# Performance work log

Measured on AMD Instinct MI355X. Metric: run time of the kernel, lower is better.

Reference implementation:

```python
import jax, jax.numpy as jnp
import numpy as np

DIM = 192
NUM_HEADS = 6
KSZ = 7
MLP_RATIO = 4.0
LEVELS = 8
EPS = 1e-5


def layernorm(x, w, b):
    mu = jnp.mean(x, axis=-1, keepdims=True)
    var = jnp.mean(jnp.square(x - mu), axis=-1, keepdims=True)
    return (x - mu) * jax.lax.rsqrt(var + EPS) * w + b


def na2d(x, qkv_w, qkv_b, proj_w, proj_b, rpb):
    # Neighborhood attention 2D with relative position bias (NATTEN semantics:
    # window of KSZ x KSZ keys per query, clamped to stay inside the image).
    B, H, W, C = x.shape
    nh, hd = NUM_HEADS, C // NUM_HEADS
    scale = hd ** -0.5
    qkv = (x @ qkv_w.T + qkv_b).reshape(B, H, W, 3, nh, hd)
    q = qkv[..., 0, :, :] * scale  # [B,H,W,nh,hd]
    k = qkv[..., 1, :, :]
    v = qkv[..., 2, :, :]

    si = jnp.clip(jnp.arange(H) - KSZ // 2, 0, H - KSZ)
    idx_i = si[:, None] + jnp.arange(KSZ)  # [H,KSZ] row indices of each window
    sj = jnp.clip(jnp.arange(W) - KSZ // 2, 0, W - KSZ)
    idx_j = sj[:, None] + jnp.arange(KSZ)  # [W,KSZ]

    def gather_win(t):  # [B,H,W,nh,hd] -> [B,H,KSZ,W,KSZ,nh,hd]
        t = jnp.take(t, idx_i.reshape(-1), axis=1).reshape(B, H, KSZ, W, nh, hd)
        t = jnp.take(t, idx_j.reshape(-1), axis=3).reshape(B, H, KSZ, W, KSZ, nh, hd)
        return t

    kw = gather_win(k)
    vw = gather_win(v)

    # scores over the KSZ x KSZ neighborhood
    scores = jnp.einsum('bxynd,bxiyjnd->bxynij', q, kw)  # [B,H,W,nh,KSZ,KSZ]

    # relative position bias: rpb is [nh, 2K-1, 2K-1]
    rel_i = idx_i - jnp.arange(H)[:, None] + (KSZ - 1)  # [H,KSZ] in [0,2K-2]
    rel_j = idx_j - jnp.arange(W)[:, None] + (KSZ - 1)  # [W,KSZ]
    bias = rpb[:, rel_i][:, :, :, rel_j]  # [nh,H,KSZ,W,KSZ]
    scores = scores + bias.transpose(1, 3, 0, 2, 4)[None]

    attn = jax.nn.softmax(scores.reshape(B, H, W, nh, KSZ * KSZ), axis=-1)
    attn = attn.reshape(B, H, W, nh, KSZ, KSZ)
    out = jnp.einsum('bxynij,bxiyjnd->bxynd', attn, vw).reshape(B, H, W, C)
    return out @ proj_w.T + proj_b


def setup_inputs() -> dict:
    key = jax.random.key(0)
    ks = jax.random.split(key, 8)
    C = DIM
    hidden = int(C * MLP_RATIO)
    init = lambda k, shape: (jax.random.normal(k, shape, dtype=jnp.float32) * 0.02)
    return {
        'x': jax.random.normal(ks[0], (1, 128, 128, C), dtype=jnp.float32),
        'qkv_w': init(ks[1], (3 * C, C)),
        'qkv_b': jnp.zeros((3 * C,), jnp.float32),
        'proj_w': init(ks[2], (C, C)),
        'proj_b': jnp.zeros((C,), jnp.float32),
        'rpb': init(ks[3], (NUM_HEADS, 2 * KSZ - 1, 2 * KSZ - 1)),
        'ln1_w': jnp.ones((C,), jnp.float32),
        'ln1_b': jnp.zeros((C,), jnp.float32),
        'ln2_w': jnp.ones((C,), jnp.float32),
        'ln2_b': jnp.zeros((C,), jnp.float32),
        'fc1_w': init(ks[4], (hidden, C)),
        'fc1_b': jnp.zeros((hidden,), jnp.float32),
        'fc2_w': init(ks[5], (C, hidden)),
        'fc2_b': jnp.zeros((C,), jnp.float32),
        'gamma1': jnp.ones((LEVELS, C), jnp.float32),
        'gamma2': jnp.ones((LEVELS, C), jnp.float32),
        'quality': 4,
    }


def reference(x, qkv_w, qkv_b, proj_w, proj_b, rpb, ln1_w, ln1_b, ln2_w, ln2_b,
              fc1_w, fc1_b, fc2_w, fc2_b, gamma1, gamma2, quality):
    # eval-mode quality gating; quality is an integer so l = quality % 1 == 0
    s = int(quality) - 1
    g1 = jnp.abs(gamma1[s])
    g2 = jnp.abs(gamma2[s])

    shortcut = x
    h = layernorm(x, ln1_w, ln1_b)
    a = na2d(h, qkv_w, qkv_b, proj_w, proj_b, rpb)
    x = shortcut + g1 * a
    h2 = layernorm(x, ln2_w, ln2_b)
    m = jax.nn.gelu(h2 @ fc1_w.T + fc1_b, approximate=False) @ fc2_w.T + fc2_b
    x = x + g2 * m
    return x
```

## Files before the change

kernel.cpp:

```cpp
#include <hip/hip_runtime.h>
#include <hip/hip_bf16.h>
#include <math.h>

#define DIM 192
#define NHD 6
#define HD 32
#define KSZ 7
#define HID 768
#define IMH 128
#define IMW 128
#define NPIX (IMH*IMW)
#define WIN 14
#define KPAD 40

typedef __attribute__((ext_vector_type(8))) short short8;
typedef __attribute__((ext_vector_type(4))) float f32x4;

#define LDS_SYNC() do { \
    asm volatile("s_waitcnt lgkmcnt(0)" ::: "memory"); \
    __builtin_amdgcn_sched_barrier(0); \
    __builtin_amdgcn_s_barrier(); } while (0)

__global__ __launch_bounds__(256) void cvt_w(
    const float* __restrict__ qw, __hip_bfloat16* __restrict__ dq)
{
    int idx = blockIdx.x * 1024 + threadIdx.x * 4;
    float4 v4 = *(const float4*)(qw + idx);
    union { ushort4 u; __hip_bfloat16 h[4]; } o;
    o.h[0] = __float2bfloat16(v4.x); o.h[1] = __float2bfloat16(v4.y);
    o.h[2] = __float2bfloat16(v4.z); o.h[3] = __float2bfloat16(v4.w);
    *(ushort4*)&dq[idx] = o.u;
}

__device__ __forceinline__ void gl_lds16(const void* g, void* l) {
    __builtin_amdgcn_global_load_lds(
        (const __attribute__((address_space(1))) void*)g,
        (__attribute__((address_space(3))) void*)l, 16, 0, 0);
}

__device__ __forceinline__ short8 cvt8(float4 a, float4 b) {
    union { short8 v; __hip_bfloat16 h[8]; } u;
    u.h[0] = __float2bfloat16(a.x); u.h[1] = __float2bfloat16(a.y);
    u.h[2] = __float2bfloat16(a.z); u.h[3] = __float2bfloat16(a.w);
    u.h[4] = __float2bfloat16(b.x); u.h[5] = __float2bfloat16(b.y);
    u.h[6] = __float2bfloat16(b.z); u.h[7] = __float2bfloat16(b.w);
    return u.v;
}

__device__ __forceinline__ void stage_rows(const __hip_bfloat16* __restrict__ src,
                                           char* ldsbase, int wave, int lane) {
    int c0 = wave * 96 + lane;
    int r0 = c0 / 24, k0 = c0 - r0 * 24;
    gl_lds16(src + (size_t)r0 * DIM + ((k0 ^ (r0 & 7)) * 8), ldsbase + (wave * 96) * 16);
    int c1 = wave * 96 + 64 + (lane & 31);
    int r1 = c1 / 24, k1 = c1 - r1 * 24;
    if (lane < 32)
        gl_lds16(src + (size_t)r1 * DIM + ((k1 ^ (r1 & 7)) * 8), ldsbase + (wave * 96 + 64) * 16);
}
__device__ __forceinline__ void stage_w2(const __hip_bfloat16* __restrict__ W2, int ch,
                                         char* ldsbase, int wave, int lane) {
    int i0 = wave * 96 + lane;
    int r0 = i0 >> 3, o0 = i0 & 7;
    gl_lds16(W2 + (size_t)r0 * HID + ch * 64 + ((o0 ^ (r0 & 7)) * 8), ldsbase + (wave * 96) * 16);
    int i1 = wave * 96 + 64 + (lane & 31);
    int r1 = i1 >> 3, o1 = i1 & 7;
    if (lane < 32)
        gl_lds16(W2 + (size_t)r1 * HID + ch * 64 + ((o1 ^ (r1 & 7)) * 8), ldsbase + (wave * 96 + 64) * 16);
}

__global__ __launch_bounds__(256, 4) void qkv_ln_gemm(
    const float* __restrict__ x, const float* __restrict__ lnw, const float* __restrict__ lnb,
    const __hip_bfloat16* __restrict__ W, const float* __restrict__ bias,
    float* __restrict__ qb, __hip_bfloat16* __restrict__ kb, __hip_bfloat16* __restrict__ vb)
{
    __shared__ __hip_bfloat16 As[32 * 192];
    __shared__ __hip_bfloat16 Ws[64 * 192];
    int tid = threadIdx.x;
    int wave = tid >> 6, lane = tid & 63;
    int q = lane >> 4, col = lane & 15;
    int wm = (wave >> 1) * 16, wn = (wave & 1) * 32;
    int m0 = blockIdx.x * 32;

    auto stageW = [&](int ch) {
        #pragma unroll
        for (int i = 0; i < 6; i++) {
            int c = i * 256 + tid;
            int r = c / 24, kc = c - r * 24;
            gl_lds16(W + (size_t)(ch * 64 + r) * DIM + ((kc ^ (r & 7)) * 8),
                     (char*)&Ws[0] + (i * 256 + wave * 64) * 16);
        }
    };

    stageW(0);

    {
        int row = tid >> 3, sub = tid & 7;
        const float4* xr = (const float4*)(x + (size_t)(m0 + row) * DIM + sub * 24);
        float4 xa[6];
        float s = 0.f;
        #pragma unroll
        for (int i = 0; i < 6; i++) {
            xa[i] = xr[i];
            s += xa[i].x + xa[i].y + xa[i].z + xa[i].w;
        }
        s += __shfl_xor(s, 1); s += __shfl_xor(s, 2); s += __shfl_xor(s, 4);
        float mu = s * (1.0f / DIM);
        float qs = 0.f;
        #pragma unroll
        for (int i = 0; i < 6; i++) {
            float a = xa[i].x - mu, b = xa[i].y - mu, c = xa[i].z - mu, d = xa[i].w - mu;
            qs += a * a + b * b + c * c + d * d;
        }
        qs += __shfl_xor(qs, 1); qs += __shfl_xor(qs, 2); qs += __shfl_xor(qs, 4);
        float rstd = rsqrtf(qs * (1.0f / DIM) + 1e-5f);
        const float4* wv = (const float4*)(lnw + sub * 24);
        const float4* bv = (const float4*)(lnb + sub * 24);
        #pragma unroll
        for (int j = 0; j < 3; j++) {
            float4 v0 = xa[j * 2], v1 = xa[j * 2 + 1];
            float4 w0 = wv[j * 2], w1 = wv[j * 2 + 1];
            float4 b0 = bv[j * 2], b1 = bv[j * 2 + 1];
            float4 o0, o1;
            o0.x = (v0.x - mu) * rstd * w0.x + b0.x;
            o0.y = (v0.y - mu) * rstd * w0.y + b0.y;
            o0.z = (v0.z - mu) * rstd * w0.z + b0.z;
            o0.w = (v0.w - mu) * rstd * w0.w + b0.w;
            o1.x = (v1.x - mu) * rstd * w1.x + b1.x;
            o1.y = (v1.y - mu) * rstd * w1.y + b1.y;
            o1.z = (v1.z - mu) * rstd * w1.z + b1.z;
            o1.w = (v1.w - mu) * rstd * w1.w + b1.w;
            int oct = sub * 3 + j;
            *(short8*)&As[row * 192 + ((oct ^ (row & 7)) * 8)] = cvt8(o0, o1);
        }
    }
    asm volatile("s_waitcnt vmcnt(0) lgkmcnt(0)" ::: "memory");
    __builtin_amdgcn_sched_barrier(0);
    __builtin_amdgcn_s_barrier();

    short8 af[6];
    {
        int rA = wm + col;
        #pragma unroll
        for (int ks = 0; ks < 6; ks++)
            af[ks] = *(const short8*)&As[rA * 192 + (((ks * 4 + q) ^ (rA & 7)) * 8)];
    }

    for (int ch = 0; ch < 9; ch++) {
        f32x4 acc[2] = {};
        #pragma unroll
        for (int ks = 0; ks < 6; ks++) {
            #pragma unroll
            for (int ni = 0; ni < 2; ni++) {
                int rB = wn + ni * 16 + col;
                short8 bf = *(const short8*)&Ws[rB * 192 + (((ks * 4 + q) ^ (rB & 7)) * 8)];
                acc[ni] = __builtin_amdgcn_mfma_f32_16x16x32_bf16(af[ks], bf, acc[ni], 0, 0, 0);
            }
        }
        asm volatile("s_waitcnt lgkmcnt(0)" ::: "memory");
        __builtin_amdgcn_sched_barrier(0);
        __builtin_amdgcn_s_barrier();
        if (ch < 8) stageW(ch + 1);
        #pragma unroll
        for (int ni = 0; ni < 2; ni++) {
            int n = ch * 64 + wn + ni * 16 + col;
            float bi = bias[n];
            int h18 = n >> 5;
            int sel = h18 / 6;
            int head = h18 - sel * 6;
            #pragma unroll
            for (int r4 = 0; r4 < 4; r4++) {
                int m = m0 + wm + q * 4 + r4;
                float v = acc[ni][r4] + bi;
                size_t idx = ((size_t)head * NPIX + m) * 32 + (n & 31);
                if (sel == 0)      qb[idx] = v * 0.17677669529663687f;
                else if (sel == 1) kb[idx] = __float2bfloat16(v);
                else               vb[idx] = __float2bfloat16(v);
            }
        }
        if (ch < 8) {
            asm volatile("s_waitcnt vmcnt(8)" ::: "memory");
            __builtin_amdgcn_s_barrier();
        }
    }
}

__global__ __launch_bounds__(1024, 4) void tail_fused(
    const __hip_bfloat16* __restrict__ A, const __hip_bfloat16* __restrict__ Wp,
    const float* __restrict__ pb, const float* __restrict__ resid,
    const float* __restrict__ gamma1, const float* __restrict__ ln2w, const float* __restrict__ ln2b,
    const __hip_bfloat16* __restrict__ W1, const float* __restrict__ b1,
    const __hip_bfloat16* __restrict__ W2, const float* __restrict__ b2,
    const float* __restrict__ gamma2, const int* __restrict__ quality,
    float* __restrict__ outf)
{
    __shared__ __hip_bfloat16 arena[64 * 768];
    __shared__ __hip_bfloat16 Wsb[2][64 * 192];
    __shared__ float lnred[4][64][2];
    __hip_bfloat16* Hs = arena + 36864;

    int tid = threadIdx.x;
    int wave = tid >> 6, lane = tid & 63;
    int q = lane >> 4, col = lane & 15;
    int wm = (wave >> 2) * 16, wq4 = wave & 3;
    int m0 = blockIdx.x * 64;
    int s = quality[0] - 1;

    stage_rows(A + (size_t)m0 * DIM, (char*)Hs, wave, lane);
    stage_rows(Wp, (char*)&Wsb[0][0], wave, lane);
    stage_rows(Wp + 64 * DIM, (char*)&Wsb[1][0], wave, lane);
    asm volatile("s_waitcnt vmcnt(2)" ::: "memory");
    __builtin_amdgcn_s_barrier();

    short8 afp[6];
    {
        int rA = wm + col;
        #pragma unroll
        for (int ks = 0; ks < 6; ks++)
            afp[ks] = *(const short8*)&Hs[rA * 192 + (((ks * 4 + q) ^ (rA & 7)) * 8)];
    }

    float v[3][4];
    float sm[4] = {}, sq[4] = {};
    auto proj_chunk = [&](int ch, const __hip_bfloat16* wsb) {
        f32x4 pacc = {};
        int rB = wq4 * 16 + col;
        #pragma unroll
        for (int ks = 0; ks < 6; ks++) {
            short8 bf = *(const short8*)&wsb[rB * 192 + (((ks * 4 + q) ^ (rB & 7)) * 8)];
            pacc = __builtin_amdgcn_mfma_f32_16x16x32_bf16(afp[ks], bf, pacc, 0, 0, 0);
        }
        int n = ch * 64 + wq4 * 16 + col;
        float bi = pb[n];
        float g = fabsf(gamma1[s * DIM + n]);
        #pragma unroll
        for (int r = 0; r < 4; r++) {
            int m = m0 + wm + q * 4 + r;
            v[ch][r] = resid[(size_t)m * DIM + n] + g * (pacc[r] + bi);
            sm[r] += v[ch][r]; sq[r] += v[ch][r] * v[ch][r];
        }
    };

    proj_chunk(0, &Wsb[0][0]);
    __builtin_amdgcn_s_barrier();
    stage_rows(Wp + 128 * DIM, (char*)&Wsb[0][0], wave, lane);
    asm volatile("s_waitcnt vmcnt(2)" ::: "memory");
    __builtin_amdgcn_s_barrier();
    proj_chunk(1, &Wsb[1][0]);
    __builtin_amdgcn_s_barrier();
    stage_rows(W1, (char*)&Wsb[1][0], wave, lane);
    asm volatile("s_waitcnt vmcnt(2)" ::: "memory");
    __builtin_amdgcn_s_barrier();
    proj_chunk(2, &Wsb[0][0]);

    #pragma unroll
    for (int off = 1; off <= 8; off <<= 1)
        #pragma unroll
        for (int r = 0; r < 4; r++) {
            sm[r] += __shfl_xor(sm[r], off);
            sq[r] += __shfl_xor(sq[r], off);
        }
    if (col == 0) {
        #pragma unroll
        for (int r = 0; r < 4; r++) {
            lnred[wq4][wm + q * 4 + r][0] = sm[r];
            lnred[wq4][wm + q * 4 + r][1] = sq[r];
        }
    }
    LDS_SYNC();
    float mu[4], rstd[4];
    #pragma unroll
    for (int r = 0; r < 4; r++) {
        int ml = wm + q * 4 + r;
        float smt = lnred[0][ml][0] + lnred[1][ml][0] + lnred[2][ml][0] + lnred[3][ml][0];
        float sqt = lnred[0][ml][1] + lnred[1][ml][1] + lnred[2][ml][1] + lnred[3][ml][1];
        mu[r] = smt * (1.0f / DIM);
        float var = sqt * (1.0f / DIM) - mu[r] * mu[r];
        rstd[r] = rsqrtf(var + 1e-5f);
    }
    #pragma unroll
    for (int ch = 0; ch < 3; ch++) {
        int n = ch * 64 + wq4 * 16 + col;
        float lw = ln2w[n], lb = ln2b[n];
        #pragma unroll
        for (int r = 0; r < 4; r++) {
            int ml = wm + q * 4 + r;
            Hs[ml * 192 + (((n >> 3) ^ (ml & 7)) * 8) + (n & 7)] =
                __float2bfloat16((v[ch][r] - mu[r]) * rstd[r] * lw + lb);
        }
    }
    LDS_SYNC();
    short8 af1[6];
    {
        int rowA = wm + col;
        #pragma unroll
        for (int ks = 0; ks < 6; ks++)
            af1[ks] = *(const short8*)&Hs[rowA * 192 + (((ks * 4 + q) ^ (rowA & 7)) * 8)];
    }
    LDS_SYNC();

    for (int t = 0; t < 12; t++) {
        if (t < 11) stage_rows(W1 + (size_t)(t + 1) * 64 * DIM, (char*)&Wsb[t & 1][0], wave, lane);
        else        stage_w2(W2, 0, (char*)&Wsb[1][0], wave, lane);
        asm volatile("s_waitcnt vmcnt(2)" ::: "memory");
        __builtin_amdgcn_s_barrier();
        const __hip_bfloat16* wsb = &Wsb[(t + 1) & 1][0];
        f32x4 a1 = {};
        int rB = wq4 * 16 + col;
        #pragma unroll
        for (int ks = 0; ks < 6; ks++) {
            short8 bf = *(const short8*)&wsb[rB * 192 + (((ks * 4 + q) ^ (rB & 7)) * 8)];
            a1 = __builtin_amdgcn_mfma_f32_16x16x32_bf16(af1[ks], bf, a1, 0, 0, 0);
        }
        int n = t * 64 + wq4 * 16 + col;
        float bi = b1[n];
        int oct = n >> 3;
        #pragma unroll
        for (int r4 = 0; r4 < 4; r4++) {
            int row = wm + q * 4 + r4;
            float vv = a1[r4] + bi;
            float u = 0.7978845608f * (vv + 0.044715f * vv * vv * vv);
            float tt = 1.f - 2.f / (__expf(2.f * u) + 1.f);
            vv = 0.5f * vv * (1.f + tt);
            int osw = (oct & ~7) | ((oct ^ row) & 7);
            *(__hip_bfloat16*)((char*)arena + row * 1536 + osw * 16 + (n & 7) * 2) =
                __float2bfloat16(vv);
        }
        __builtin_amdgcn_s_barrier();
    }
    LDS_SYNC();

    f32x4 acc2[3] = {};
    for (int ch = 0; ch < 12; ch++) {
        if (ch < 11) {
            stage_w2(W2, ch + 1, (char*)&Wsb[ch & 1][0], wave, lane);
            asm volatile("s_waitcnt vmcnt(2)" ::: "memory");
        } else {
            asm volatile("s_waitcnt vmcnt(0)" ::: "memory");
        }
        __builtin_amdgcn_s_barrier();
        const __hip_bfloat16* wsb = &Wsb[(ch + 1) & 1][0];
        #pragma unroll
        for (int ks = 0; ks < 2; ks++) {
            int row = wm + col;
            int og = ch * 8 + ks * 4 + q;
            int osw = (og & ~7) | ((og ^ row) & 7);
            short8 a2 = *(const short8*)((char*)arena + row * 1536 + osw * 16);
            #pragma unroll
            for (int f = 0; f < 3; f++) {
                int rB = f * 64 + wq4 * 16 + col;
                short8 bf = *(const short8*)&wsb[rB * 64 + (((ks * 4 + q) ^ (rB & 7)) * 8)];
                acc2[f] = __builtin_amdgcn_mfma_f32_16x16x32_bf16(a2, bf, acc2[f], 0, 0, 0);
            }
        }
        __builtin_amdgcn_s_barrier();
    }

    #pragma unroll
    for (int f = 0; f < 3; f++) {
        int n = f * 64 + wq4 * 16 + col;
        float g = fabsf(gamma2[s * DIM + n]);
        float bi = b2[n];
        #pragma unroll
        for (int r4 = 0; r4 < 4; r4++) {
            int m = m0 + wm + q * 4 + r4;
            outf[(size_t)m * DIM + n] = v[f][r4] + g * (acc2[f][r4] + bi);
        }
    }
}

__device__ __forceinline__ void unpack8(const __hip_bfloat16* ptr, float* f) {
    short8 s8 = *(const short8*)ptr;
    union { short8 v; unsigned u[4]; } c; c.v = s8;
    #pragma unroll
    for (int w = 0; w < 4; w++) {
        f[2*w]   = __uint_as_float(c.u[w] << 16);
        f[2*w+1] = __uint_as_float(c.u[w] & 0xffff0000u);
    }
}

__global__ __launch_bounds__(256, 4) void attn_kernel3(
    const float* __restrict__ qbuf, const __hip_bfloat16* __restrict__ kbuf,
    const __hip_bfloat16* __restrict__ vbuf, const float* __restrict__ rpb,
    __hip_bfloat16* __restrict__ out,
    const float* __restrict__ pw, const float* __restrict__ f1w, const float* __restrict__ f2w,
    __hip_bfloat16* __restrict__ dp, __hip_bfloat16* __restrict__ df1, __hip_bfloat16* __restrict__ df2)
{
    if (blockIdx.x >= 256) {
        if (blockIdx.y != 0) return;
        int blk = blockIdx.x - 256, t = threadIdx.x;
        const float* s; __hip_bfloat16* d; int base;
        if (blk < 36)       { s = pw;  d = dp;  base = blk * 1024; }
        else if (blk < 180) { s = f1w; d = df1; base = (blk - 36) * 1024; }
        else                { s = f2w; d = df2; base = (blk - 180) * 1024; }
        int idx = base + t * 4;
        float4 v4 = *(const float4*)(s + idx);
        union { ushort4 u; __hip_bfloat16 h[4]; } o;
        o.h[0] = __float2bfloat16(v4.x); o.h[1] = __float2bfloat16(v4.y);
        o.h[2] = __float2bfloat16(v4.z); o.h[3] = __float2bfloat16(v4.w);
        *(ushort4*)&d[idx] = o.u;
        return;
    }

    __shared__ __hip_bfloat16 Ks[WIN * WIN * KPAD];
    __shared__ __hip_bfloat16 Vs[WIN * WIN * KPAD];
    __shared__ float rpbs[169];

    int head = blockIdx.y;
    int tile = blockIdx.x;
    int ti0 = (tile >> 4) * 8;
    int tj0 = (tile & 15) * 8;
    int wi0 = ti0 - 3; wi0 = wi0 < 0 ? 0 : (wi0 > IMH - WIN ? IMH - WIN : wi0);
    int wj0 = tj0 - 3; wj0 = wj0 < 0 ? 0 : (wj0 > IMW - WIN ? IMW - WIN : wj0);

    int tid = threadIdx.x;
    const size_t hbase = (size_t)head * NPIX;

    for (int c = tid; c < 784; c += 256) {
        int i = c / 56, part = c - i * 56;
        int n = i * WIN + (part >> 2);
        int dp2 = part & 3;
        size_t goff = (hbase + (size_t)(wi0 + i) * IMW + wj0) * 32 + part * 8;
        short8 kk = *(const short8*)(kbuf + goff);
        short8 vv = *(const short8*)(vbuf + goff);
        *(short8*)&Ks[n * KPAD + dp2 * 8] = kk;
        *(short8*)&Vs[n * KPAD + dp2 * 8] = vv;
    }
    if (tid < 169) rpbs[tid] = rpb[head * 169 + tid];

    int p   = tid >> 2;
    int sub = tid & 3;
    int pi = ti0 + (p >> 3), pj = tj0 + (p & 7);
    int si = pi - 3; si = si < 0 ? 0 : (si > IMH - KSZ ? IMH - KSZ : si);
    int sj = pj - 3; sj = sj < 0 ? 0 : (sj > IMW - KSZ ? IMW - KSZ : sj);
    int bi = si - wi0, bj = sj - wj0;

    const float4* qp = (const float4*)(qbuf + (hbase + (size_t)(pi * IMW + pj)) * 32 + sub * 8);
    float4 q0 = qp[0], q1 = qp[1];
    float q[8] = {q0.x, q0.y, q0.z, q0.w, q1.x, q1.y, q1.z, q1.w};

    __syncthreads();

    float m = -1e30f, l = 0.f;
    float acc[8] = {};
    #pragma unroll
    for (int ki = 0; ki < KSZ; ki++) {
        int rbase = (bi + ki) * WIN + bj;
        const float* rb = &rpbs[(si + ki - pi + 6) * 13 + (sj - pj + 6)];
        float s7[KSZ];
        #pragma unroll
        for (int kj = 0; kj < KSZ; kj++) {
            float kf[8];
            unpack8(&Ks[(rbase + kj) * KPAD + sub * 8], kf);
            float d = q[0]*kf[0] + q[1]*kf[1] + q[2]*kf[2] + q[3]*kf[3]
                    + q[4]*kf[4] + q[5]*kf[5] + q[6]*kf[6] + q[7]*kf[7];
            d += __shfl_xor(d, 1);
            d += __shfl_xor(d, 2);
            s7[kj] = d + rb[kj];
        }
        float rmax = s7[0];
        #pragma unroll
        for (int kj = 1; kj < KSZ; kj++) rmax = fmaxf(rmax, s7[kj]);
        float mn = fmaxf(m, rmax);
        float co = __expf(m - mn);
        l *= co;
        #pragma unroll
        for (int e = 0; e < 8; e++) acc[e] *= co;
        #pragma unroll
        for (int kj = 0; kj < KSZ; kj++) {
            float pw2 = __expf(s7[kj] - mn);
            l += pw2;
            float vf[8];
            unpack8(&Vs[(rbase + kj) * KPAD + sub * 8], vf);
            #pragma unroll
            for (int e = 0; e < 8; e++) acc[e] += pw2 * vf[e];
        }
        m = mn;
    }
    float rl = 1.f / l;
    __hip_bfloat16* op = out + (size_t)(pi * IMW + pj) * DIM + head * HD + sub * 8;
    #pragma unroll
    for (int e = 0; e < 8; e++) op[e] = __float2bfloat16(acc[e] * rl);
}

extern "C" void kernel_launch(void* const* d_in, const int* in_sizes, int n_in,
                              void* d_out, int out_size, void* d_ws, size_t ws_size,
                              hipStream_t stream)
{
    const float* x      = (const float*)d_in[0];
    const float* qkv_w  = (const float*)d_in[1];
    const float* qkv_b  = (const float*)d_in[2];
    const float* proj_w = (const float*)d_in[3];
    const float* proj_b = (const float*)d_in[4];
    const float* rpb    = (const float*)d_in[5];
    const float* ln1_w  = (const float*)d_in[6];
    const float* ln1_b  = (const float*)d_in[7];
    const float* ln2_w  = (const float*)d_in[8];
    const float* ln2_b  = (const float*)d_in[9];
    const float* fc1_w  = (const float*)d_in[10];
    const float* fc1_b  = (const float*)d_in[11];
    const float* fc2_w  = (const float*)d_in[12];
    const float* fc2_b  = (const float*)d_in[13];
    const float* gamma1 = (const float*)d_in[14];
    const float* gamma2 = (const float*)d_in[15];
    const int*   quality= (const int*)d_in[16];
    float* out = (float*)d_out;

    char* ws = (char*)d_ws;
    float*          qbuf   = (float*)ws;
    __hip_bfloat16* kbuf   = (__hip_bfloat16*)(ws + 12582912);
    __hip_bfloat16* vbuf   = (__hip_bfloat16*)(ws + 18874368);
    __hip_bfloat16* attn_b = (__hip_bfloat16*)(ws + 44040192);
    __hip_bfloat16* wq     = (__hip_bfloat16*)(ws + 50331648);
    __hip_bfloat16* wp     = (__hip_bfloat16*)(ws + 50552832);
    __hip_bfloat16* wf1    = (__hip_bfloat16*)(ws + 50626560);
    __hip_bfloat16* wf2    = (__hip_bfloat16*)(ws + 50921472);

    cvt_w<<<108, 256, 0, stream>>>(qkv_w, wq);
    qkv_ln_gemm<<<512, 256, 0, stream>>>(
        x, ln1_w, ln1_b, wq, qkv_b, qbuf, kbuf, vbuf);
    attn_kernel3<<<dim3(256 + 324, NHD), 256, 0, stream>>>(
        qbuf, kbuf, vbuf, rpb, attn_b, proj_w, fc1_w, fc2_w, wp, wf1, wf2);
    tail_fused<<<256, 1024, 0, stream>>>(
        attn_b, wp, proj_b, x, gamma1, ln2_w, ln2_b,
        wf1, fc1_b, wf2, fc2_b, gamma2, quality, out);
}
```

Baseline: 170.6 us.

## Compute neighborhood attention with dense MFMA over the tile's key window

Replaces the per-thread scalar dot-product attention with bf16 MFMA: each wave computes scores for 16 queries against all 208 padded window keys, masks out keys outside each query's 7x7 neighborhood, applies a plain softmax, and multiplies probabilities with a transposed V tile via MFMA. This moves the work from scalar FMAs and shuffles onto matrix cores. In exchange it computes about four times more scores than needed, uses more LDS (which lowers the occupancy hint), and rounds probabilities to bf16.

Result: no change. 167.8 us (-1.6%).

```diff
diff --git a/kernel.cpp b/kernel.cpp
--- a/kernel.cpp
+++ b/kernel.cpp
@@ -368,17 +368,7 @@
     }
 }
 
-__device__ __forceinline__ void unpack8(const __hip_bfloat16* ptr, float* f) {
-    short8 s8 = *(const short8*)ptr;
-    union { short8 v; unsigned u[4]; } c; c.v = s8;
-    #pragma unroll
-    for (int w = 0; w < 4; w++) {
-        f[2*w]   = __uint_as_float(c.u[w] << 16);
-        f[2*w+1] = __uint_as_float(c.u[w] & 0xffff0000u);
-    }
-}
-
-__global__ __launch_bounds__(256, 4) void attn_kernel3(
+__global__ __launch_bounds__(256, 2) void attn_mfma(
     const float* __restrict__ qbuf, const __hip_bfloat16* __restrict__ kbuf,
     const __hip_bfloat16* __restrict__ vbuf, const float* __restrict__ rpb,
     __hip_bfloat16* __restrict__ out,
@@ -401,85 +391,125 @@
         return;
     }
 
-    __shared__ __hip_bfloat16 Ks[WIN * WIN * KPAD];
-    __shared__ __hip_bfloat16 Vs[WIN * WIN * KPAD];
+    __shared__ __hip_bfloat16 Ks[208 * 40];
+    __shared__ __hip_bfloat16 Vt[32 * 228];
+    __shared__ __hip_bfloat16 Ps[4][16 * 232];
     __shared__ float rpbs[169];
 
-    int head = blockIdx.y;
-    int tile = blockIdx.x;
-    int ti0 = (tile >> 4) * 8;
-    int tj0 = (tile & 15) * 8;
+    int head = blockIdx.y, tile = blockIdx.x;
+    int ti0 = (tile >> 4) * 8, tj0 = (tile & 15) * 8;
     int wi0 = ti0 - 3; wi0 = wi0 < 0 ? 0 : (wi0 > IMH - WIN ? IMH - WIN : wi0);
     int wj0 = tj0 - 3; wj0 = wj0 < 0 ? 0 : (wj0 > IMW - WIN ? IMW - WIN : wj0);
-
     int tid = threadIdx.x;
     const size_t hbase = (size_t)head * NPIX;
 
     for (int c = tid; c < 784; c += 256) {
         int i = c / 56, part = c - i * 56;
         int n = i * WIN + (part >> 2);
-        int dp2 = part & 3;
+        int d0 = (part & 3) * 8;
         size_t goff = (hbase + (size_t)(wi0 + i) * IMW + wj0) * 32 + part * 8;
         short8 kk = *(const short8*)(kbuf + goff);
         short8 vv = *(const short8*)(vbuf + goff);
-        *(short8*)&Ks[n * KPAD + dp2 * 8] = kk;
-        *(short8*)&Vs[n * KPAD + dp2 * 8] = vv;
+        *(short8*)&Ks[n * 40 + d0] = kk;
+        union { short8 v; unsigned short u[8]; } cu; cu.v = vv;
+        #pragma unroll
+        for (int e = 0; e < 8; e++)
+            *(unsigned short*)&Vt[(d0 + e) * 228 + n] = cu.u[e];
+    }
+    for (int c = tid; c < 896; c += 256) {
+        int d = c / 28, k = 196 + (c - d * 28);
+        *(unsigned short*)&Vt[d * 228 + k] = 0;
     }
     if (tid < 169) rpbs[tid] = rpb[head * 169 + tid];
 
-    int p   = tid >> 2;
-    int sub = tid & 3;
-    int pi = ti0 + (p >> 3), pj = tj0 + (p & 7);
-    int si = pi - 3; si = si < 0 ? 0 : (si > IMH - KSZ ? IMH - KSZ : si);
-    int sj = pj - 3; sj = sj < 0 ? 0 : (sj > IMW - KSZ ? IMW - KSZ : sj);
-    int bi = si - wi0, bj = sj - wj0;
-
-    const float4* qp = (const float4*)(qbuf + (hbase + (size_t)(pi * IMW + pj)) * 32 + sub * 8);
-    float4 q0 = qp[0], q1 = qp[1];
-    float q[8] = {q0.x, q0.y, q0.z, q0.w, q1.x, q1.y, q1.z, q1.w};
+    int w = tid >> 6, l = tid & 63;
+    int cl = l & 15, ch = l >> 4;
+    #pragma unroll
+    for (int j = 0; j < 4; j++)
+        *(unsigned short*)&Ps[w][cl * 232 + 208 + ch * 4 + j] = 0;
+
+    int p0 = w * 16 + cl;
+    int qpi = ti0 + (p0 >> 3), qpj = tj0 + (p0 & 7);
+    const float4* qp = (const float4*)(qbuf + (hbase + (size_t)(qpi * IMW + qpj)) * 32 + ch * 8);
+    short8 afq = cvt8(qp[0], qp[1]);
+
+    int pi_r[4], pj_r[4], si_r[4], sj_r[4];
+    #pragma unroll
+    for (int r = 0; r < 4; r++) {
+        int qr = w * 16 + ch * 4 + r;
+        int pi = ti0 + (qr >> 3), pj = tj0 + (qr & 7);
+        int si = pi - 3; si = si < 0 ? 0 : (si > IMH - KSZ ? IMH - KSZ : si);
+        int sj = pj - 3; sj = sj < 0 ? 0 : (sj > IMW - KSZ ? IMW - KSZ : sj);
+        pi_r[r] = pi; pj_r[r] = pj; si_r[r] = si; sj_r[r] = sj;
+    }
 
     __syncthreads();
 
-    float m = -1e30f, l = 0.f;
-    float acc[8] = {};
-    #pragma unroll
-    for (int ki = 0; ki < KSZ; ki++) {
-        int rbase = (bi + ki) * WIN + bj;
-        const float* rb = &rpbs[(si + ki - pi + 6) * 13 + (sj - pj + 6)];
-        float s7[KSZ];
-        #pragma unroll
-        for (int kj = 0; kj < KSZ; kj++) {
-            float kf[8];
-            unpack8(&Ks[(rbase + kj) * KPAD + sub * 8], kf);
-            float d = q[0]*kf[0] + q[1]*kf[1] + q[2]*kf[2] + q[3]*kf[3]
-                    + q[4]*kf[4] + q[5]*kf[5] + q[6]*kf[6] + q[7]*kf[7];
-            d += __shfl_xor(d, 1);
-            d += __shfl_xor(d, 2);
-            s7[kj] = d + rb[kj];
-        }
-        float rmax = s7[0];
-        #pragma unroll
-        for (int kj = 1; kj < KSZ; kj++) rmax = fmaxf(rmax, s7[kj]);
-        float mn = fmaxf(m, rmax);
-        float co = __expf(m - mn);
-        l *= co;
-        #pragma unroll
-        for (int e = 0; e < 8; e++) acc[e] *= co;
-        #pragma unroll
-        for (int kj = 0; kj < KSZ; kj++) {
-            float pw2 = __expf(s7[kj] - mn);
-            l += pw2;
-            float vf[8];
-            unpack8(&Vs[(rbase + kj) * KPAD + sub * 8], vf);
-            #pragma unroll
-            for (int e = 0; e < 8; e++) acc[e] += pw2 * vf[e];
-        }
-        m = mn;
-    }
-    float rl = 1.f / l;
-    __hip_bfloat16* op = out + (size_t)(pi * IMW + pj) * DIM + head * HD + sub * 8;
-    #pragma unroll
-    for (int e = 0; e < 8; e++) op[e] = __float2bfloat16(acc[e] * rl);
+    f32x4 sc[13] = {};
+    #pragma unroll
+    for (int t = 0; t < 13; t++) {
+        short8 bk = *(const short8*)&Ks[(t * 16 + cl) * 40 + ch * 8];
+        sc[t] = __builtin_amdgcn_mfma_f32_16x16x32_bf16(afq, bk, sc[t], 0, 0, 0);
+    }
+
+    float mrow[4] = {-1e30f, -1e30f, -1e30f, -1e30f};
+    #pragma unroll
+    for (int t = 0; t < 13; t++) {
+        int n = t * 16 + cl;
+        int ni = (n * 9363) >> 17;
+        int nj = n - ni * 14;
+        int gi = wi0 + ni, gj = wj0 + nj;
+        #pragma unroll
+        for (int r = 0; r < 4; r++) {
+            int di = gi - si_r[r], dj = gj - sj_r[r];
+            bool valid = ((unsigned)di < 7u) && ((unsigned)dj < 7u);
+            int bix = (gi - pi_r[r] + 6) * 13 + (gj - pj_r[r] + 6);
+            float b = rpbs[valid ? bix : 0];
+            float sv = valid ? sc[t][r] + b : -1e30f;
+            sc[t][r] = sv;
+            mrow[r] = fmaxf(mrow[r], sv);
+        }
+    }
+    #pragma unroll
+    for (int off = 1; off <= 8; off <<= 1)
+        #pragma unroll
+        for (int r = 0; r < 4; r++) mrow[r] = fmaxf(mrow[r], __shfl_xor(mrow[r], off));
+
+    float lrow[4] = {};
+    #pragma unroll
+    for (int t = 0; t < 13; t++) {
+        #pragma unroll
+        for (int r = 0; r < 4; r++) {
+            float e = __expf(sc[t][r] - mrow[r]);
+            lrow[r] += e;
+            Ps[w][(ch * 4 + r) * 232 + t * 16 + cl] = __float2bfloat16(e);
+        }
+    }
+    #pragma unroll
+    for (int off = 1; off <= 8; off <<= 1)
+        #pragma unroll
+        for (int r = 0; r < 4; r++) lrow[r] += __shfl_xor(lrow[r], off);
+
+    f32x4 o[2] = {};
+    #pragma unroll
+    for (int ks = 0; ks < 7; ks++) {
+        short8 ap = *(const short8*)&Ps[w][cl * 232 + ks * 32 + ch * 8];
+        #pragma unroll
+        for (int nt = 0; nt < 2; nt++) {
+            short8 bv = *(const short8*)&Vt[(nt * 16 + cl) * 228 + ks * 32 + ch * 8];
+            o[nt] = __builtin_amdgcn_mfma_f32_16x16x32_bf16(ap, bv, o[nt], 0, 0, 0);
+        }
+    }
+
+    #pragma unroll
+    for (int r = 0; r < 4; r++) {
+        int qr = w * 16 + ch * 4 + r;
+        int pi = ti0 + (qr >> 3), pj = tj0 + (qr & 7);
+        float rl = 1.f / lrow[r];
+        __hip_bfloat16* op = out + (size_t)(pi * IMW + pj) * DIM + head * HD;
+        op[cl]      = __float2bfloat16(o[0][r] * rl);
+        op[16 + cl] = __float2bfloat16(o[1][r] * rl);
+    }
 }
 
 extern "C" void kernel_launch(void* const* d_in, const int* in_sizes, int n_in,
@@ -518,7 +548,7 @@
     cvt_w<<<108, 256, 0, stream>>>(qkv_w, wq);
     qkv_ln_gemm<<<512, 256, 0, stream>>>(
         x, ln1_w, ln1_b, wq, qkv_b, qbuf, kbuf, vbuf);
-    attn_kernel3<<<dim3(256 + 324, NHD), 256, 0, stream>>>(
+    attn_mfma<<<dim3(256 + 324, NHD), 256, 0, stream>>>(
         qbuf, kbuf, vbuf, rpb, attn_b, proj_w, fc1_w, fc2_w, wp, wf1, wf2);
     tail_fused<<<256, 1024, 0, stream>>>(
         attn_b, wp, proj_b, x, gamma1, ln2_w, ln2_b,
```
